# Kernel tuning notes

Measured on AMD Instinct MI355X. Metric: run time of the kernel, lower is better.

Reference implementation:

```python
import jax, jax.numpy as jnp
import numpy as np

B, CIN, COUT, K, L = 32, 128, 128, 7, 4096
STRIDE, PAD = 1, 3
TEMP = 1.0


def setup_inputs() -> dict:
    key = jax.random.key(0)
    k1, k2 = jax.random.split(key)
    x = jax.random.normal(k1, (B, CIN, L), dtype=jnp.float32)
    weight = jax.random.normal(k2, (COUT, CIN, K), dtype=jnp.float32) * 0.1  # init: normal(0, 0.1)
    bias = jnp.zeros((COUT,), dtype=jnp.float32)
    return {"x": x, "weight": weight, "bias": bias}


def reference(x, weight, bias):
    # Soft tropical conv (intended math of the module):
    #   y[b,o,w] = T * logsumexp_{c,k}( (x[b,c,w*stride+k] + W[o,c,k]) / T ) + bias[o]
    # with -inf padding (exp(-inf)=0 => plain zero padding in exp space).
    # Computed as a numerically-stabilized standard conv in exp space, which is
    # mathematically identical and avoids materializing the (B,O,C,K,L) tensor.
    xm = jnp.max(x)
    wm = jnp.max(weight)
    ex = jnp.exp((x - xm) / TEMP)          # (B, CIN, L)
    ew = jnp.exp((weight - wm) / TEMP)     # (COUT, CIN, K)
    s = jax.lax.conv_general_dilated(
        ex, ew,
        window_strides=(STRIDE,),
        padding=[(PAD, PAD)],
        dimension_numbers=("NCH", "OIH", "NCH"),
    )  # (B, COUT, L_out); cross-correlation, matching torch unfold indexing x[i+k]
    y = TEMP * jnp.log(s) + (xm + wm)
    return y + bias[None, :, None]
```

## Files before the change

### kernel.cpp

```cpp
#include <hip/hip_runtime.h>
#include <hip/hip_bf16.h>
#include <cstdint>
#include <cstddef>

#define B_N   32
#define CIN_  128
#define COUT_ 128
#define KW_   7
#define L_    4096
#define NW_   256
#define NWELEM (KW_ * COUT_ * CIN_)

#define SX_ROWS  264
#define SX_ELEMS (SX_ROWS * CIN_)

typedef __attribute__((ext_vector_type(8))) short  bf16x8;
typedef __attribute__((ext_vector_type(4))) float  f32x4;

__global__ __launch_bounds__(256) void prep_w_kernel(
        const float* __restrict__ w, __hip_bfloat16* __restrict__ ewb) {
    int base = blockIdx.x * 1024 + threadIdx.x;
    #pragma unroll
    for (int i = 0; i < 4; ++i) {
        int idx = base + 256 * i;
        int e  = idx & 7;
        int li = (idx >> 3) & 63;
        int cc = (idx >> 9) & 3;
        int blk = idx >> 11;
        int og = blk & 7, t = blk >> 3;
        int o  = og * 16 + (li & 15);
        int ch = cc * 32 + ((li >> 4) << 3) + e;
        ewb[idx] = __float2bfloat16(__expf(w[(o * CIN_ + ch) * KW_ + t]));
    }
}

__global__ __launch_bounds__(256, 2) void tropconv_kernel(
        const float* __restrict__ x,
        const __hip_bfloat16* __restrict__ ewb,
        const float* __restrict__ bias,
        float* __restrict__ out) {
    __shared__ __align__(16) __hip_bfloat16 sX[SX_ELEMS];

    const int tid  = threadIdx.x;
    const int lane = tid & 63;
    const int wave = tid >> 6;
    const int wm   = wave >> 1;
    const int wn   = wave & 1;
    const int l15  = lane & 15;
    const int q    = lane >> 4;

    const int b  = blockIdx.y;
    const int w0 = blockIdx.x * NW_;
    const float* xb = x + (size_t)b * CIN_ * L_;

    #pragma unroll
    for (int i = 0; i < 8; ++i) {
        int idx = tid + 256 * i;
        int c   = idx >> 4;
        int gb  = idx & 15;
        int cHi = c >> 3, cLo = c & 7;
        #pragma unroll
        for (int j = 0; j < 5; ++j) {
            int g = gb + 16 * j;
            if (g >= 66) continue;
            int l0  = w0 - 4 + 4 * g;
            int l0c = min(max(l0, 0), L_ - 4);
            f32x4 v = *(const f32x4*)(xb + (size_t)c * L_ + l0c);
            #pragma unroll
            for (int e = 0; e < 4; ++e) {
                int l = l0 + e;
                int p = 4 * g + e - 1;
                if ((unsigned)p < 262u) {
                    float val = ((unsigned)l < (unsigned)L_) ? __expf(v[e]) : 0.0f;
                    int slot = cHi ^ ((p ^ (p >> 2)) & 7);
                    sX[(p << 7) + (slot << 3) + cLo] = __float2bfloat16(val);
                }
            }
        }
    }

    f32x4 acc[4][8];
    #pragma unroll
    for (int i = 0; i < 4; ++i)
        #pragma unroll
        for (int j = 0; j < 8; ++j)
            acc[i][j] = (f32x4){0.f, 0.f, 0.f, 0.f};

    __syncthreads();

#define ALOAD(AF, T, CC)                                                     \
    do {                                                                     \
        _Pragma("unroll")                                                    \
        for (int mi = 0; mi < 4; ++mi)                                       \
            AF[mi] = *(const bf16x8*)&ewb[(((((T) * 8 + wm * 4 + mi) * 4     \
                                             + (CC)) << 6) + lane) * 8];     \
    } while (0)

#define BDOT(AF, T, CC)                                                      \
    do {                                                                     \
        bf16x8 bx[8];                                                        \
        _Pragma("unroll")                                                    \
        for (int ni = 0; ni < 8; ++ni) {                                     \
            int p = wn * 128 + ni * 16 + l15 + (T);                          \
            int g = ((CC) * 4 + q) ^ ((p ^ (p >> 2)) & 7);                   \
            bx[ni] = *(const bf16x8*)&sX[(p << 7) + (g << 3)];               \
        }                                                                    \
        __builtin_amdgcn_s_setprio(1);                                       \
        _Pragma("unroll")                                                    \
        for (int mi = 0; mi < 4; ++mi)                                       \
            _Pragma("unroll")                                                \
            for (int ni = 0; ni < 8; ++ni)                                   \
                acc[mi][ni] = __builtin_amdgcn_mfma_f32_16x16x32_bf16(       \
                    AF[mi], bx[ni], acc[mi][ni], 0, 0, 0);                   \
        __builtin_amdgcn_s_setprio(0);                                       \
    } while (0)

    {
        bf16x8 afA[4], afB[4];
        ALOAD(afA, 0, 0);
        ALOAD(afB, 1, 0);  BDOT(afA, 0, 0);
        ALOAD(afA, 2, 0);  BDOT(afB, 1, 0);
        ALOAD(afB, 3, 0);  BDOT(afA, 2, 0);
        ALOAD(afA, 4, 0);  BDOT(afB, 3, 0);
        ALOAD(afB, 5, 0);  BDOT(afA, 4, 0);
        ALOAD(afA, 6, 0);  BDOT(afB, 5, 0);
        ALOAD(afB, 0, 1);  BDOT(afA, 6, 0);
        ALOAD(afA, 1, 1);  BDOT(afB, 0, 1);
        ALOAD(afB, 2, 1);  BDOT(afA, 1, 1);
        ALOAD(afA, 3, 1);  BDOT(afB, 2, 1);
        ALOAD(afB, 4, 1);  BDOT(afA, 3, 1);
        ALOAD(afA, 5, 1);  BDOT(afB, 4, 1);
        ALOAD(afB, 6, 1);  BDOT(afA, 5, 1);
        ALOAD(afA, 0, 2);  BDOT(afB, 6, 1);
        ALOAD(afB, 1, 2);  BDOT(afA, 0, 2);
        ALOAD(afA, 2, 2);  BDOT(afB, 1, 2);
        ALOAD(afB, 3, 2);  BDOT(afA, 2, 2);
        ALOAD(afA, 4, 2);  BDOT(afB, 3, 2);
        ALOAD(afB, 5, 2);  BDOT(afA, 4, 2);
        ALOAD(afA, 6, 2);  BDOT(afB, 5, 2);
        ALOAD(afB, 0, 3);  BDOT(afA, 6, 2);
        ALOAD(afA, 1, 3);  BDOT(afB, 0, 3);
        ALOAD(afB, 2, 3);  BDOT(afA, 1, 3);
        ALOAD(afA, 3, 3);  BDOT(afB, 2, 3);
        ALOAD(afB, 4, 3);  BDOT(afA, 3, 3);
        ALOAD(afA, 5, 3);  BDOT(afB, 4, 3);
        ALOAD(afB, 6, 3);  BDOT(afA, 5, 3);
                           BDOT(afB, 6, 3);
    }
#undef ALOAD
#undef BDOT

    float* outb = out + (size_t)b * COUT_ * L_;
    #pragma unroll
    for (int mi = 0; mi < 4; ++mi) {
        #pragma unroll
        for (int r = 0; r < 4; ++r) {
            int o = wm * 64 + mi * 16 + q * 4 + r;
            float bv = bias[o];
            #pragma unroll
            for (int ni = 0; ni < 8; ++ni) {
                int w = w0 + wn * 128 + ni * 16 + l15;
                outb[(size_t)o * L_ + w] = __logf(acc[mi][ni][r]) + bv;
            }
        }
    }
}

extern "C" void kernel_launch(void* const* d_in, const int* in_sizes, int n_in,
                              void* d_out, int out_size, void* d_ws, size_t ws_size,
                              hipStream_t stream) {
    const float* x    = (const float*)d_in[0];
    const float* wgt  = (const float*)d_in[1];
    const float* bias = (const float*)d_in[2];
    float* out = (float*)d_out;

    __hip_bfloat16* ewb = (__hip_bfloat16*)d_ws;

    prep_w_kernel<<<NWELEM / 1024, 256, 0, stream>>>(wgt, ewb);
    tropconv_kernel<<<dim3(L_ / NW_, B_N), 256, 0, stream>>>(x, ewb, bias, out);
}
```

Before: 176.0 us.

## Stage x transpose through swizzled shared tile to vectorize sX writes

New measurement: 169.2 us. 3.8% less time.

```diff
diff --git a/kernel.cpp b/kernel.cpp
--- a/kernel.cpp
+++ b/kernel.cpp
@@ -40,6 +40,7 @@
         const float* __restrict__ bias,
         float* __restrict__ out) {
     __shared__ __align__(16) __hip_bfloat16 sX[SX_ELEMS];
+    __shared__ __align__(16) __hip_bfloat16 tileT[32 * 136];
 
     const int tid  = threadIdx.x;
     const int lane = tid & 63;
@@ -53,30 +54,45 @@
     const int w0 = blockIdx.x * NW_;
     const float* xb = x + (size_t)b * CIN_ * L_;
 
-    #pragma unroll
-    for (int i = 0; i < 8; ++i) {
-        int idx = tid + 256 * i;
-        int c   = idx >> 4;
-        int gb  = idx & 15;
-        int cHi = c >> 3, cLo = c & 7;
+    for (int k = 0; k < 9; ++k) {
+        const int lo = k << 5;
+        const int nr = (k == 8) ? 6 : 32;
         #pragma unroll
-        for (int j = 0; j < 5; ++j) {
-            int g = gb + 16 * j;
-            if (g >= 66) continue;
-            int l0  = w0 - 4 + 4 * g;
-            int l0c = min(max(l0, 0), L_ - 4);
-            f32x4 v = *(const f32x4*)(xb + (size_t)c * L_ + l0c);
-            #pragma unroll
-            for (int e = 0; e < 4; ++e) {
-                int l = l0 + e;
-                int p = 4 * g + e - 1;
-                if ((unsigned)p < 262u) {
-                    float val = ((unsigned)l < (unsigned)L_) ? __expf(v[e]) : 0.0f;
-                    int slot = cHi ^ ((p ^ (p >> 2)) & 7);
-                    sX[(p << 7) + (slot << 3) + cLo] = __float2bfloat16(val);
+        for (int it = 0; it < 8; ++it) {
+            int gid = tid + 256 * it;
+            int c   = gid >> 4;
+            int gq  = gid & 15;
+            if (gq < 9) {
+                int lx  = w0 - 4 + lo + (gq << 2);
+                int lxc = min(max(lx, 0), L_ - 4);
+                f32x4 v = *(const f32x4*)(xb + (size_t)c * L_ + lxc);
+                #pragma unroll
+                for (int e = 0; e < 4; ++e) {
+                    int p  = lo + (gq << 2) + e - 1;
+                    int pl = p - lo;
+                    if ((unsigned)pl < (unsigned)nr) {
+                        int lg = lx + e;
+                        float val = ((unsigned)lg < (unsigned)L_) ? __expf(v[e]) : 0.0f;
+                        int sw = (pl >> 2) & 15;
+                        tileT[pl * 136 + (c ^ (sw << 3))] = __float2bfloat16(val);
+                    }
                 }
             }
         }
+        __syncthreads();
+        #pragma unroll
+        for (int it = 0; it < 2; ++it) {
+            int gid   = tid + 256 * it;
+            int l_loc = gid >> 4;
+            int gc    = gid & 15;
+            if (l_loc < nr) {
+                int sw = (l_loc >> 2) & 15;
+                bf16x8 vv = *(const bf16x8*)&tileT[l_loc * 136 + ((gc ^ sw) << 3)];
+                int p = lo + l_loc;
+                *(bf16x8*)&sX[(p << 7) + ((gc ^ (p & 7)) << 3)] = vv;
+            }
+        }
+        __syncthreads();
     }
 
     f32x4 acc[4][8];
@@ -85,8 +101,6 @@
         #pragma unroll
         for (int j = 0; j < 8; ++j)
             acc[i][j] = (f32x4){0.f, 0.f, 0.f, 0.f};
-
-    __syncthreads();
 
 #define ALOAD(AF, T, CC)                                                     \
     do {                                                                     \
@@ -102,7 +116,7 @@
         _Pragma("unroll")                                                    \
         for (int ni = 0; ni < 8; ++ni) {                                     \
             int p = wn * 128 + ni * 16 + l15 + (T);                          \
-            int g = ((CC) * 4 + q) ^ ((p ^ (p >> 2)) & 7);                   \
+            int g = ((CC) * 4 + q) ^ (p & 7);                                \
             bx[ni] = *(const bf16x8*)&sX[(p << 7) + (g << 3)];               \
         }                                                                    \
         __builtin_amdgcn_s_setprio(1);                                       \
```
